# Kernel optimization log

Hardware: AMD Instinct MI355X
Metric: run time of the kernel (lower is better)

The kernel has to match this reference:

```python
import jax, jax.numpy as jnp
import numpy as np

B, S, HID = 2, 2048, 4096
NH, NKV, D = 32, 8, 128  # heads, kv heads, head_dim
GROUPS = NH // NKV
THETA = 10000.0


def _rope_tables():
    inv_freq = 1.0 / (THETA ** (np.arange(0, D, 2, dtype=np.float32) / D))
    pos = np.arange(S, dtype=np.float32)
    freqs = pos[:, None] * inv_freq[None, :]          # [S, D/2]
    emb = np.concatenate([freqs, freqs], axis=-1)      # [S, D]
    cos = np.broadcast_to(np.cos(emb)[None], (B, S, D)).copy()
    sin = np.broadcast_to(np.sin(emb)[None], (B, S, D)).copy()
    return jnp.asarray(cos), jnp.asarray(sin)


def setup_inputs() -> dict:
    key = jax.random.key(0)
    ks = jax.random.split(key, 5)
    hidden_states = jax.random.normal(ks[0], (B, S, HID), dtype=jnp.float32)
    cos, sin = _rope_tables()
    std = 0.02
    Wq = jax.random.normal(ks[1], (NH * D, HID), dtype=jnp.float32) * std
    Wk = jax.random.normal(ks[2], (NKV * D, HID), dtype=jnp.float32) * std
    Wv = jax.random.normal(ks[3], (NKV * D, HID), dtype=jnp.float32) * std
    Wo = jax.random.normal(ks[4], (HID, NH * D), dtype=jnp.float32) * std
    return {"hidden_states": hidden_states, "cos": cos, "sin": sin,
            "Wq": Wq, "Wk": Wk, "Wv": Wv, "Wo": Wo}


def _rotate_half(x):
    x1, x2 = jnp.split(x, 2, axis=-1)
    return jnp.concatenate([-x2, x1], axis=-1)


def reference(hidden_states, cos, sin, Wq, Wk, Wv, Wo):
    b, s, _ = hidden_states.shape
    # QKV projections (no bias; attention_bias=False)
    q = (hidden_states @ Wq.T).reshape(b, s, NH, D).transpose(0, 2, 1, 3)    # [B,NH,S,D]
    k = (hidden_states @ Wk.T).reshape(b, s, NKV, D).transpose(0, 2, 1, 3)   # [B,NKV,S,D]
    v = (hidden_states @ Wv.T).reshape(b, s, NKV, D).transpose(0, 2, 1, 3)
    # RoPE (HF apply_rotary_pos_emb: cos/sin unsqueezed at head dim)
    c = cos[:, None, :, :]
    sn = sin[:, None, :, :]
    q = q * c + _rotate_half(q) * sn
    k = k * c + _rotate_half(k) * sn
    # GQA repeat_kv
    k = jnp.repeat(k, GROUPS, axis=1)                                        # [B,NH,S,D]
    v = jnp.repeat(v, GROUPS, axis=1)
    # dense evalmode: scores + causal mask + fp32 softmax
    scores = jnp.einsum('bhqd,bhkd->bhqk', q, k) / jnp.sqrt(jnp.float32(D))
    causal = jnp.triu(jnp.ones((s, s), dtype=bool), k=1)                     # True above diag
    scores = jnp.where(causal[None, None], jnp.float32(-jnp.inf), scores)
    attn = jax.nn.softmax(scores.astype(jnp.float32), axis=-1).astype(v.dtype)
    out = jnp.einsum('bhqk,bhkd->bhqd', attn, v)                             # [B,NH,S,D]
    out = out.transpose(0, 2, 1, 3).reshape(b, s, NH * D)
    return out @ Wo.T
```

## Files before the change

### kernel.cpp

```cpp
#include <hip/hip_runtime.h>
#include <hip/hip_bf16.h>

#define DEV __device__ __forceinline__

typedef __attribute__((ext_vector_type(8))) short bf16x8;
typedef __attribute__((ext_vector_type(4))) short s16x4;
typedef __attribute__((ext_vector_type(4))) float f32x4;

constexpr int B_ = 2, S_ = 2048, HID_ = 4096, NH_ = 32, NKV_ = 8, D_ = 128;
constexpr int GROUPS_ = NH_ / NKV_;
constexpr float QSCALE_ = 0.08838834764831845f * 1.4426950408889634f;

DEV unsigned short f2bf(float x) {
    union { float f; unsigned int u; } v; v.f = x;
    unsigned int r = v.u + 0x7fffu + ((v.u >> 16) & 1u);
    return (unsigned short)(r >> 16);
}

DEV f32x4 mfma16(bf16x8 a, bf16x8 b, f32x4 c) {
    return __builtin_amdgcn_mfma_f32_16x16x32_bf16(a, b, c, 0, 0, 0);
}

DEV void gll16(const void* g, void* l) {
    __builtin_amdgcn_global_load_lds(
        (const __attribute__((address_space(1))) unsigned int*)g,
        (__attribute__((address_space(3))) unsigned int*)l, 16, 0, 0);
}

__global__ __launch_bounds__(256) void cast_all_k(
    const float* __restrict__ s0, const float* __restrict__ s1,
    const float* __restrict__ s2, const float* __restrict__ s3,
    const float* __restrict__ s4,
    unsigned short* __restrict__ d0, unsigned short* __restrict__ d1,
    unsigned short* __restrict__ d2, unsigned short* __restrict__ d3,
    unsigned short* __restrict__ d4)
{
    int bb = blockIdx.x;
    const float* s; unsigned short* d; int off;
    if      (bb < 8192)  { s = s0; d = d0; off = bb; }
    else if (bb < 16384) { s = s1; d = d1; off = bb - 8192; }
    else if (bb < 18432) { s = s2; d = d2; off = bb - 16384; }
    else if (bb < 20480) { s = s3; d = d3; off = bb - 18432; }
    else                 { s = s4; d = d4; off = bb - 20480; }
    size_t i = ((size_t)off * 256 + threadIdx.x) * 8;
    const f32x4* sp = (const f32x4*)(s + i);
    f32x4 a = sp[0], b = sp[1];
    bf16x8 o;
    o[0] = (short)f2bf(a[0]); o[1] = (short)f2bf(a[1]);
    o[2] = (short)f2bf(a[2]); o[3] = (short)f2bf(a[3]);
    o[4] = (short)f2bf(b[0]); o[5] = (short)f2bf(b[1]);
    o[6] = (short)f2bf(b[2]); o[7] = (short)f2bf(b[3]);
    *(bf16x8*)(d + i) = o;
}

template<int EPI>
__global__ __launch_bounds__(512, 2) void gemm256_k(
    const unsigned short* __restrict__ A, const unsigned short* __restrict__ Bw,
    float* __restrict__ Cf, unsigned short* __restrict__ Qo,
    const float* __restrict__ cosT, const float* __restrict__ sinT,
    int M, int N, int K)
{
    __shared__ __align__(16) unsigned short lds[65536];
    const int tid = threadIdx.x, lane = tid & 63;
    const int w = tid >> 6, wm = w >> 2, wn = w & 3;
    const int la = lane & 15, lb = lane >> 4;

    const int nwg = (int)gridDim.x;
    const int cpx = nwg >> 3;
    const int bid = (int)blockIdx.x;
    const int sw = (bid & 7) * cpx + (bid >> 3);
    const int ntn = N >> 8;
    const int bm = (sw / ntn) << 8, bn = (sw % ntn) << 8;

    const int srow = tid >> 3;
    const int scol8 = (tid & 7) ^ (srow & 7);
    const size_t rK = (size_t)K;
    const unsigned short* gA = A + (size_t)(bm + srow) * rK + scol8 * 8;
    const unsigned short* gB = Bw + (size_t)(bn + srow) * rK + scol8 * 8;

#define STAGE_A_H0(buf, kt) { gll16(gA + (size_t)(kt),            &lds[(buf)*16384 + tid*8]); \
                              gll16(gA + (size_t)(kt) + 128*rK,   &lds[(buf)*16384 + 8192 + tid*8]); }
#define STAGE_A_H1(buf, kt) { gll16(gA + (size_t)(kt) + 64*rK,    &lds[(buf)*16384 + 4096 + tid*8]); \
                              gll16(gA + (size_t)(kt) + 192*rK,   &lds[(buf)*16384 + 12288 + tid*8]); }
#define STAGE_B_H0(buf, kt) { gll16(gB + (size_t)(kt),            &lds[32768 + (buf)*16384 + tid*8]); \
                              gll16(gB + (size_t)(kt) + 64*rK,    &lds[32768 + (buf)*16384 + 4096 + tid*8]); }
#define STAGE_B_H1(buf, kt) { gll16(gB + (size_t)(kt) + 128*rK,   &lds[32768 + (buf)*16384 + 8192 + tid*8]); \
                              gll16(gB + (size_t)(kt) + 192*rK,   &lds[32768 + (buf)*16384 + 12288 + tid*8]); }
#define SB0() __builtin_amdgcn_sched_barrier(0)

    f32x4 acc[8][4];
#pragma unroll
    for (int m = 0; m < 8; ++m)
#pragma unroll
        for (int j = 0; j < 4; ++j) acc[m][j] = f32x4{0.f, 0.f, 0.f, 0.f};

    auto rdA = [&](int buf, int m, int kk) -> bf16x8 {
        int r = wm * 128 + m * 16 + la;
        int slot = (kk * 4 + lb) ^ (la & 7);
        return *(const bf16x8*)&lds[buf * 16384 + r * 64 + slot * 8];
    };
    auto rdB = [&](int buf, int j, int kk) -> bf16x8 {
        int r = (wn + 4 * j) * 16 + la;
        int slot = (kk * 4 + lb) ^ (la & 7);
        return *(const bf16x8*)&lds[32768 + buf * 16384 + r * 64 + slot * 8];
    };

    STAGE_A_H0(0, 0); STAGE_B_H0(0, 0); STAGE_B_H1(0, 0); STAGE_A_H1(0, 0);

    bf16x8 af[4][2], b01[2][2], b23[2][2];
    int cur = 0;
    const int nt = K >> 6;
    for (int t = 0; t < nt; ++t) {
        const bool pre = (t + 1 < nt);
        const int kn = (t + 1) << 6;
        const int nb = cur ^ 1;
        asm volatile("s_waitcnt vmcnt(2)" ::: "memory");
        SB0(); __builtin_amdgcn_s_barrier(); SB0();
#pragma unroll
        for (int m = 0; m < 4; ++m)
#pragma unroll
            for (int kk = 0; kk < 2; ++kk) af[m][kk] = rdA(cur, m, kk);
#pragma unroll
        for (int j = 0; j < 2; ++j)
#pragma unroll
            for (int kk = 0; kk < 2; ++kk) b01[j][kk] = rdB(cur, j, kk);
        if (pre) STAGE_A_H0(nb, kn);
        __builtin_amdgcn_s_setprio(1);
#pragma unroll
        for (int kk = 0; kk < 2; ++kk)
#pragma unroll
            for (int m = 0; m < 4; ++m)
#pragma unroll
                for (int j = 0; j < 2; ++j)
                    acc[m][j] = mfma16(af[m][kk], b01[j][kk], acc[m][j]);
        __builtin_amdgcn_s_setprio(0);
        SB0(); __builtin_amdgcn_s_barrier(); SB0();
#pragma unroll
        for (int j = 0; j < 2; ++j)
#pragma unroll
            for (int kk = 0; kk < 2; ++kk) b23[j][kk] = rdB(cur, j + 2, kk);
        if (pre) STAGE_B_H0(nb, kn);
        __builtin_amdgcn_s_setprio(1);
#pragma unroll
        for (int kk = 0; kk < 2; ++kk)
#pragma unroll
            for (int m = 0; m < 4; ++m)
#pragma unroll
                for (int j = 0; j < 2; ++j)
                    acc[m][j + 2] = mfma16(af[m][kk], b23[j][kk], acc[m][j + 2]);
        __builtin_amdgcn_s_setprio(0);
        if (pre) { asm volatile("s_waitcnt vmcnt(4)" ::: "memory"); }
        else     { asm volatile("s_waitcnt vmcnt(0)" ::: "memory"); }
        SB0(); __builtin_amdgcn_s_barrier(); SB0();
#pragma unroll
        for (int m = 0; m < 4; ++m)
#pragma unroll
            for (int kk = 0; kk < 2; ++kk) af[m][kk] = rdA(cur, m + 4, kk);
        if (pre) STAGE_B_H1(nb, kn);
        __builtin_amdgcn_s_setprio(1);
#pragma unroll
        for (int kk = 0; kk < 2; ++kk)
#pragma unroll
            for (int m = 0; m < 4; ++m)
#pragma unroll
                for (int j = 0; j < 2; ++j)
                    acc[m + 4][j + 2] = mfma16(af[m][kk], b23[j][kk], acc[m + 4][j + 2]);
        __builtin_amdgcn_s_setprio(0);
        SB0(); __builtin_amdgcn_s_barrier(); SB0();
        if (pre) STAGE_A_H1(nb, kn);
        __builtin_amdgcn_s_setprio(1);
#pragma unroll
        for (int kk = 0; kk < 2; ++kk)
#pragma unroll
            for (int m = 0; m < 4; ++m)
#pragma unroll
                for (int j = 0; j < 2; ++j)
                    acc[m + 4][j] = mfma16(af[m][kk], b01[j][kk], acc[m + 4][j]);
        __builtin_amdgcn_s_setprio(0);
        cur ^= 1;
    }
#undef STAGE_A_H0
#undef STAGE_A_H1
#undef STAGE_B_H0
#undef STAGE_B_H1

    const int srow0 = bm + wm * 128;
    if constexpr (EPI == 0) {
#pragma unroll
        for (int m = 0; m < 8; ++m)
#pragma unroll
            for (int j = 0; j < 4; ++j) {
                int col = bn + (wn + 4 * j) * 16 + la;
#pragma unroll
                for (int r = 0; r < 4; ++r)
                    Cf[(size_t)(srow0 + m * 16 + lb * 4 + r) * N + col] = acc[m][j][r];
            }
    } else {
        const int hbase = bn >> 7;
        const int d = wn * 16 + la;
#pragma unroll
        for (int m = 0; m < 8; ++m) {
#pragma unroll
            for (int r = 0; r < 4; ++r) {
                int row = srow0 + m * 16 + lb * 4 + r;
                float cv = cosT[(size_t)row * D_ + d];
                float sv = sinT[(size_t)row * D_ + d];
#pragma unroll
                for (int p = 0; p < 2; ++p) {
                    float x1 = acc[m][p * 2 + 0][r], x2 = acc[m][p * 2 + 1][r];
                    unsigned short* o = Qo + (size_t)row * (NH_ * D_) + (hbase + p) * D_ + d;
                    o[0]  = f2bf((x1 * cv - x2 * sv) * QSCALE_);
                    o[64] = f2bf((x2 * cv + x1 * sv) * QSCALE_);
                }
            }
        }
    }
}

__global__ __launch_bounds__(512, 4) void gemm_kv_k(
    const unsigned short* __restrict__ A, const unsigned short* __restrict__ Bw,
    unsigned short* __restrict__ Ko, unsigned short* __restrict__ Vo,
    const float* __restrict__ cosT, const float* __restrict__ sinT,
    int M, int K)
{
    __shared__ __align__(16) unsigned short lds[32768];
    const int tid = threadIdx.x, lane = tid & 63;
    const int w = tid >> 6, wm = w >> 2, wn = w & 3;
    const int la = lane & 15, lb = lane >> 4;

    const int nwg = (int)gridDim.x;
    const int cpx = nwg >> 3;
    const int bid = (int)blockIdx.x;
    const int sw = (bid & 7) * cpx + (bid >> 3);
    const int ntn = 2048 >> 7;
    const int bm = (sw / ntn) << 7, bn = (sw % ntn) << 7;

    const int srow = tid >> 3;
    const int scol8 = (tid & 7) ^ (srow & 7);
    const size_t rK = (size_t)K;
    const unsigned short* gA = A + (size_t)(bm + srow) * rK + scol8 * 8;
    const unsigned short* gB = Bw + (size_t)(bn + srow) * rK + scol8 * 8;

#define KV_STG_A(buf, kt)  { gll16(gA + (size_t)(kt),          &lds[(buf)*8192 + tid*8]); \
                             gll16(gA + (size_t)(kt) + 64*rK,  &lds[(buf)*8192 + 4096 + tid*8]); }
#define KV_STG_B0(buf, kt)   gll16(gB + (size_t)(kt),          &lds[16384 + (buf)*8192 + tid*8])
#define KV_STG_B1(buf, kt)   gll16(gB + (size_t)(kt) + 64*rK,  &lds[16384 + (buf)*8192 + 4096 + tid*8])
#define SB0() __builtin_amdgcn_sched_barrier(0)

    f32x4 acc[4][2];
#pragma unroll
    for (int m = 0; m < 4; ++m)
#pragma unroll
        for (int j = 0; j < 2; ++j) acc[m][j] = f32x4{0.f, 0.f, 0.f, 0.f};

    auto rdA = [&](int buf, int m, int kk) -> bf16x8 {
        int r = wm * 64 + m * 16 + la;
        int slot = (kk * 4 + lb) ^ (la & 7);
        return *(const bf16x8*)&lds[buf * 8192 + r * 64 + slot * 8];
    };
    auto rdB = [&](int buf, int j, int kk) -> bf16x8 {
        int r = (wn + 4 * j) * 16 + la;
        int slot = (kk * 4 + lb) ^ (la & 7);
        return *(const bf16x8*)&lds[16384 + buf * 8192 + r * 64 + slot * 8];
    };

    KV_STG_A(0, 0); KV_STG_B0(0, 0); KV_STG_B1(0, 0);

    bf16x8 af[4][2], bf0[2], bf1[2];
    int cur = 0;
    const int nt = K >> 6;
    for (int t = 0; t < nt; ++t) {
        const bool pre = (t + 1 < nt);
        const int kn = (t + 1) << 6;
        const int nb = cur ^ 1;
        asm volatile("s_waitcnt vmcnt(1)" ::: "memory");
        SB0(); __builtin_amdgcn_s_barrier(); SB0();
#pragma unroll
        for (int m = 0; m < 4; ++m)
#pragma unroll
            for (int kk = 0; kk < 2; ++kk) af[m][kk] = rdA(cur, m, kk);
#pragma unroll
        for (int kk = 0; kk < 2; ++kk) bf0[kk] = rdB(cur, 0, kk);
        if (pre) { KV_STG_A(nb, kn); KV_STG_B0(nb, kn); }
        __builtin_amdgcn_s_setprio(1);
#pragma unroll
        for (int kk = 0; kk < 2; ++kk)
#pragma unroll
            for (int m = 0; m < 4; ++m)
                acc[m][0] = mfma16(af[m][kk], bf0[kk], acc[m][0]);
        __builtin_amdgcn_s_setprio(0);
        if (pre) { asm volatile("s_waitcnt vmcnt(3)" ::: "memory"); }
        else     { asm volatile("s_waitcnt vmcnt(0)" ::: "memory"); }
        SB0(); __builtin_amdgcn_s_barrier(); SB0();
#pragma unroll
        for (int kk = 0; kk < 2; ++kk) bf1[kk] = rdB(cur, 1, kk);
        if (pre) KV_STG_B1(nb, kn);
        __builtin_amdgcn_s_setprio(1);
#pragma unroll
        for (int kk = 0; kk < 2; ++kk)
#pragma unroll
            for (int m = 0; m < 4; ++m)
                acc[m][1] = mfma16(af[m][kk], bf1[kk], acc[m][1]);
        __builtin_amdgcn_s_setprio(0);
        cur ^= 1;
    }
#undef KV_STG_A
#undef KV_STG_B0
#undef KV_STG_B1
#undef SB0

    const int rbase = bm + wm * 64;
    if (bn < 1024) {
        const int hbase = bn >> 7;
        const int d = wn * 16 + la;
#pragma unroll
        for (int m = 0; m < 4; ++m)
#pragma unroll
            for (int r = 0; r < 4; ++r) {
                int row = rbase + m * 16 + lb * 4 + r;
                float cv = cosT[(size_t)row * D_ + d];
                float sv = sinT[(size_t)row * D_ + d];
                float x1 = acc[m][0][r], x2 = acc[m][1][r];
                unsigned short* o = Ko + (size_t)row * (NKV_ * D_) + hbase * D_ + d;
                o[0]  = f2bf(x1 * cv - x2 * sv);
                o[64] = f2bf(x2 * cv + x1 * sv);
            }
    } else {
        const int kv = (bn - 1024) >> 7;
#pragma unroll
        for (int m = 0; m < 4; ++m) {
            int row = rbase + m * 16 + lb * 4;
            int b = row >> 11, s = row & (S_ - 1);
#pragma unroll
            for (int j = 0; j < 2; ++j) {
                int d = (wn + 4 * j) * 16 + la;
                s16x4 pk;
#pragma unroll
                for (int r = 0; r < 4; ++r) pk[r] = (short)f2bf(acc[m][j][r]);
                *(s16x4*)&Vo[((size_t)(b * NKV_ + kv) * D_ + d) * S_ + s] = pk;
            }
        }
    }
}

template<int EPI, bool ABF16>
__global__ __launch_bounds__(256) void gemm_legacy_k(
    const void* __restrict__ Ap, const float* __restrict__ Bp,
    void* __restrict__ Cp, const float* __restrict__ cosT,
    const float* __restrict__ sinT, int M, int N, int K, float scale)
{
    constexpr int LDT = 40;
    __shared__ __align__(16) unsigned short Asm[128 * LDT];
    __shared__ __align__(16) unsigned short Bsm[128 * LDT];
    const int tid = threadIdx.x;
    const int lane = tid & 63;
    const int w = tid >> 6;
    const int la = lane & 15, lb = lane >> 4;
    const int ntn = N >> 7;
    const int bm = (int)(blockIdx.x / ntn) << 7;
    const int bn = (int)(blockIdx.x % ntn) << 7;

    f32x4 acc[2][8];
#pragma unroll
    for (int i = 0; i < 2; ++i)
#pragma unroll
        for (int j = 0; j < 8; ++j) acc[i][j] = f32x4{0.f, 0.f, 0.f, 0.f};

    for (int kt = 0; kt < K; kt += 32) {
        if constexpr (!ABF16) {
#pragma unroll
            for (int it = 0; it < 4; ++it) {
                int idx = it * 256 + tid;
                int r = idx >> 3, c = (idx & 7) << 2;
                const float* g = (const float*)Ap + (size_t)(bm + r) * K + kt + c;
                f32x4 v = *(const f32x4*)g;
                union { unsigned long long q; unsigned short u[4]; } pk;
                pk.u[0] = f2bf(v[0]); pk.u[1] = f2bf(v[1]);
                pk.u[2] = f2bf(v[2]); pk.u[3] = f2bf(v[3]);
                *(unsigned long long*)&Asm[r * LDT + c] = pk.q;
            }
        } else {
#pragma unroll
            for (int it = 0; it < 2; ++it) {
                int idx = it * 256 + tid;
                int r = idx >> 2, c = (idx & 3) << 3;
                const unsigned short* g =
                    (const unsigned short*)Ap + (size_t)(bm + r) * K + kt + c;
                *(bf16x8*)&Asm[r * LDT + c] = *(const bf16x8*)g;
            }
        }
#pragma unroll
        for (int it = 0; it < 4; ++it) {
            int idx = it * 256 + tid;
            int r = idx >> 3, c = (idx & 7) << 2;
            const float* g = Bp + (size_t)(bn + r) * K + kt + c;
            f32x4 v = *(const f32x4*)g;
            union { unsigned long long q; unsigned short u[4]; } pk;
            pk.u[0] = f2bf(v[0]); pk.u[1] = f2bf(v[1]);
            pk.u[2] = f2bf(v[2]); pk.u[3] = f2bf(v[3]);
            *(unsigned long long*)&Bsm[r * LDT + c] = pk.q;
        }
        __syncthreads();
        bf16x8 af0 = *(bf16x8*)&Asm[(w * 32 + la) * LDT + lb * 8];
        bf16x8 af1 = *(bf16x8*)&Asm[(w * 32 + 16 + la) * LDT + lb * 8];
#pragma unroll
        for (int nb = 0; nb < 8; ++nb) {
            bf16x8 bfr = *(bf16x8*)&Bsm[(nb * 16 + la) * LDT + lb * 8];
            acc[0][nb] = mfma16(af0, bfr, acc[0][nb]);
            acc[1][nb] = mfma16(af1, bfr, acc[1][nb]);
        }
        __syncthreads();
    }

    const int rbase = bm + w * 32;
    if constexpr (EPI == 0) {
        float* C = (float*)Cp;
#pragma unroll
        for (int mf = 0; mf < 2; ++mf)
#pragma unroll
            for (int nb = 0; nb < 8; ++nb)
#pragma unroll
                for (int r = 0; r < 4; ++r)
                    C[(size_t)(rbase + mf * 16 + lb * 4 + r) * N + bn + nb * 16 + la] =
                        acc[mf][nb][r];
    } else if constexpr (EPI == 1) {
        unsigned short* C = (unsigned short*)Cp;
#pragma unroll
        for (int mf = 0; mf < 2; ++mf) {
#pragma unroll
            for (int r = 0; r < 4; ++r) {
                int m = rbase + mf * 16 + lb * 4 + r;
                const float* cb = cosT + (size_t)m * D_;
                const float* sb = sinT + (size_t)m * D_;
#pragma unroll
                for (int nb = 0; nb < 4; ++nb) {
                    int d = nb * 16 + la;
                    float c = cb[d], s = sb[d];
                    float x1 = acc[mf][nb][r], x2 = acc[mf][nb + 4][r];
                    C[(size_t)m * N + bn + d]      = f2bf((x1 * c - x2 * s) * scale);
                    C[(size_t)m * N + bn + d + 64] = f2bf((x2 * c + x1 * s) * scale);
                }
            }
        }
    } else {
        unsigned short* C = (unsigned short*)Cp;
#pragma unroll
        for (int mf = 0; mf < 2; ++mf)
#pragma unroll
            for (int nb = 0; nb < 8; ++nb)
#pragma unroll
                for (int r = 0; r < 4; ++r) {
                    int m = rbase + mf * 16 + lb * 4 + r;
                    int b = m >> 11, s = m & (S_ - 1);
                    int n = bn + nb * 16 + la;
                    int kv = n >> 7, d = n & 127;
                    C[(((size_t)b * NKV_ + kv) * D_ + d) * S_ + s] =
                        f2bf(acc[mf][nb][r]);
                }
    }
}

__global__ __launch_bounds__(256, 2) void attn3_k(
    const unsigned short* __restrict__ Qw,
    const unsigned short* __restrict__ Kw,
    const unsigned short* __restrict__ Vt,
    unsigned short* __restrict__ Ow)
{
    __shared__ __align__(16) unsigned short Ksm[2][64 * 128];
    __shared__ __align__(16) unsigned short Vsm[2][128 * 64];
    const int tid = threadIdx.x, lane = tid & 63, w = tid >> 6;
    const int la = lane & 15, lb = lane >> 4;
    const int blk = blockIdx.x;
    const int qbi = (S_ / 128 - 1) - (blk >> 6);
    const int bh = blk & 63;
    const int b = bh >> 5, h = bh & 31;
    const int kvh = h >> 2;
    const int qb = qbi * 128;
    const int qw0 = qb + w * 32;

    bf16x8 fq[2][4];
    const unsigned short* qp =
        Qw + ((size_t)(b * S_ + qw0 + la) * NH_ + h) * D_ + lb * 8;
#pragma unroll
    for (int mq = 0; mq < 2; ++mq)
#pragma unroll
        for (int kc = 0; kc < 4; ++kc)
            fq[mq][kc] = *(const bf16x8*)(qp + (size_t)mq * 16 * NH_ * D_ + kc * 32);

    float m_[2], l_[2];
    f32x4 oacc[8][2];
    m_[0] = m_[1] = -__builtin_inff();
    l_[0] = l_[1] = 0.f;
#pragma unroll
    for (int db = 0; db < 8; ++db)
#pragma unroll
        for (int mq = 0; mq < 2; ++mq) oacc[db][mq] = f32x4{0.f, 0.f, 0.f, 0.f};

    const int krb = tid >> 4, ksl = tid & 15;
    const int vrb = tid >> 3, vsl = tid & 7;
    const unsigned short* kbase = Kw + ((size_t)b * S_ * NKV_ + kvh) * D_;
    const unsigned short* vbase = Vt + ((size_t)(b * NKV_ + kvh) * D_) * S_;

#define STAGE_KV(buf, kv0) {                                                   \
    _Pragma("unroll")                                                          \
    for (int it = 0; it < 4; ++it) {                                           \
        int row = it * 16 + krb;                                               \
        int cc = ksl ^ (row & 7);                                              \
        gll16(kbase + (size_t)(kv0 + row) * NKV_ * D_ + cc * 8,                \
              &Ksm[buf][(it * 256 + tid) * 8]);                                \
    }                                                                          \
    _Pragma("unroll")                                                          \
    for (int it = 0; it < 4; ++it) {                                           \
        int row = it * 32 + vrb;                                               \
        int cc = vsl ^ (row & 7);                                              \
        gll16(vbase + (size_t)row * S_ + (kv0) + cc * 8,                       \
              &Vsm[buf][(it * 256 + tid) * 8]);                                \
    }                                                                          \
}
#define SB0() __builtin_amdgcn_sched_barrier(0)

    STAGE_KV(0, 0);
    int cur = 0;
    const int ntiles = (qb + 128) >> 6;
    for (int t = 0; t < ntiles; ++t) {
        const int kv0 = t << 6;
        const bool pre = (t + 1 < ntiles);
        if (pre) STAGE_KV(cur ^ 1, kv0 + 64);
        if (pre) { asm volatile("s_waitcnt vmcnt(8)" ::: "memory"); }
        else     { asm volatile("s_waitcnt vmcnt(0)" ::: "memory"); }
        SB0(); __builtin_amdgcn_s_barrier(); SB0();

        if (kv0 < qw0 + 32) {
            f32x4 sacc[4][2];
#pragma unroll
            for (int nk = 0; nk < 4; ++nk)
#pragma unroll
                for (int mq = 0; mq < 2; ++mq) sacc[nk][mq] = f32x4{0.f, 0.f, 0.f, 0.f};
#pragma unroll
            for (int kc = 0; kc < 4; ++kc) {
#pragma unroll
                for (int nk = 0; nk < 4; ++nk) {
                    int row = nk * 16 + la;
                    int slot = (kc * 4 + lb) ^ (la & 7);
                    bf16x8 fk = *(const bf16x8*)&Ksm[cur][row * 128 + slot * 8];
#pragma unroll
                    for (int mq = 0; mq < 2; ++mq)
                        sacc[nk][mq] = mfma16(fk, fq[mq][kc], sacc[nk][mq]);
                }
            }
            const bool diag = (kv0 + 63 > qw0);
            float pv[4][2][4];
            float pm[2];
#pragma unroll
            for (int mq = 0; mq < 2; ++mq) {
                int q = qw0 + mq * 16 + la;
                float mx = -__builtin_inff();
#pragma unroll
                for (int nk = 0; nk < 4; ++nk)
#pragma unroll
                    for (int r = 0; r < 4; ++r) {
                        float s = sacc[nk][mq][r];
                        if (diag) {
                            int k = kv0 + nk * 16 + lb * 4 + r;
                            s = (k <= q) ? s : -__builtin_inff();
                        }
                        pv[nk][mq][r] = s;
                        mx = fmaxf(mx, s);
                    }
                mx = fmaxf(mx, __shfl_xor(mx, 16));
                mx = fmaxf(mx, __shfl_xor(mx, 32));
                pm[mq] = mx;
            }
            const bool upd =
                __any((pm[0] > m_[0] + 8.f) || (pm[1] > m_[1] + 8.f));
            if (upd) {
#pragma unroll
                for (int mq = 0; mq < 2; ++mq) {
                    float mn = fmaxf(m_[mq], pm[mq]);
                    float fac = exp2f(m_[mq] - mn);
                    m_[mq] = mn;
                    l_[mq] *= fac;
#pragma unroll
                    for (int db = 0; db < 8; ++db) oacc[db][mq] *= fac;
                }
            }
            float tsum[2] = {0.f, 0.f};
#pragma unroll
            for (int nk = 0; nk < 4; ++nk)
#pragma unroll
                for (int mq = 0; mq < 2; ++mq)
#pragma unroll
                    for (int r = 0; r < 4; ++r) {
                        float p = exp2f(pv[nk][mq][r] - m_[mq]);
                        pv[nk][mq][r] = p;
                        tsum[mq] += p;
                    }
#pragma unroll
            for (int mq = 0; mq < 2; ++mq) {
                float s = tsum[mq];
                s += __shfl_xor(s, 16);
                s += __shfl_xor(s, 32);
                l_[mq] += s;
            }
            union { bf16x8 v; __hip_bfloat162 h[4]; } fp[2][2];
#pragma unroll
            for (int mq = 0; mq < 2; ++mq)
#pragma unroll
                for (int ks = 0; ks < 2; ++ks) {
                    fp[mq][ks].h[0] = __float22bfloat162_rn(
                        float2{pv[2 * ks][mq][0], pv[2 * ks][mq][1]});
                    fp[mq][ks].h[1] = __float22bfloat162_rn(
                        float2{pv[2 * ks][mq][2], pv[2 * ks][mq][3]});
                    fp[mq][ks].h[2] = __float22bfloat162_rn(
                        float2{pv[2 * ks + 1][mq][0], pv[2 * ks + 1][mq][1]});
                    fp[mq][ks].h[3] = __float22bfloat162_rn(
                        float2{pv[2 * ks + 1][mq][2], pv[2 * ks + 1][mq][3]});
                }
            const int lbh = lb >> 1, lbo = (lb & 1) * 4;
#pragma unroll
            for (int ks = 0; ks < 2; ++ks)
#pragma unroll
                for (int db = 0; db < 8; ++db) {
                    int row = db * 16 + la;
                    int rx = row & 7;
                    const unsigned short* vb = &Vsm[cur][row * 64];
                    s16x4 v0 = *(const s16x4*)&vb[((ks * 4 + lbh) ^ rx) * 8 + lbo];
                    s16x4 v1 = *(const s16x4*)&vb[((ks * 4 + 2 + lbh) ^ rx) * 8 + lbo];
                    bf16x8 fv = __builtin_shufflevector(v0, v1, 0, 1, 2, 3, 4, 5, 6, 7);
#pragma unroll
                    for (int mq = 0; mq < 2; ++mq)
                        oacc[db][mq] = mfma16(fv, fp[mq][ks].v, oacc[db][mq]);
                }
        }
        SB0(); __builtin_amdgcn_s_barrier(); SB0();
        cur ^= 1;
    }
#undef STAGE_KV
#undef SB0

#pragma unroll
    for (int mq = 0; mq < 2; ++mq) {
        float rl = 1.f / l_[mq];
        int q = qw0 + mq * 16 + la;
#pragma unroll
        for (int db = 0; db < 8; ++db) {
            f32x4 o = oacc[db][mq];
            s16x4 pk;
#pragma unroll
            for (int r = 0; r < 4; ++r) pk[r] = (short)f2bf(o[r] * rl);
            int d = db * 16 + lb * 4;
            *(s16x4*)(Ow + (size_t)(b * S_ + q) * (NH_ * D_) + h * D_ + d) = pk;
        }
    }
}

extern "C" void kernel_launch(void* const* d_in, const int* in_sizes, int n_in,
                              void* d_out, int out_size, void* d_ws, size_t ws_size,
                              hipStream_t stream) {
    const float* hs   = (const float*)d_in[0];
    const float* cosT = (const float*)d_in[1];
    const float* sinT = (const float*)d_in[2];
    const float* Wq   = (const float*)d_in[3];
    const float* Wk   = (const float*)d_in[4];
    const float* Wv   = (const float*)d_in[5];
    const float* Wo   = (const float*)d_in[6];

    constexpr size_t Qn  = (size_t)B_ * S_ * NH_ * D_;
    constexpr size_t Kn  = (size_t)B_ * S_ * NKV_ * D_;
    constexpr size_t Hn  = (size_t)B_ * S_ * HID_;
    constexpr size_t Wqn = (size_t)NH_ * D_ * HID_;
    constexpr size_t Wkn = (size_t)NKV_ * D_ * HID_;

    unsigned short* Qws   = (unsigned short*)d_ws;
    unsigned short* Kws   = Qws + Qn;
    unsigned short* Vtws  = Kws + Kn;
    unsigned short* AOws  = Vtws + Kn;
    unsigned short* hsb   = AOws + Qn;
    unsigned short* Wqkvb = hsb + Hn;
    unsigned short* Wob   = Wqkvb + Wqn + 2 * Wkn;
    constexpr size_t need = (Qn + 2 * Kn + Qn + Hn + Wqn + 2 * Wkn + Wqn) * 2;

    const int M = B_ * S_;
    dim3 blk(256);

    if (ws_size >= need) {
        cast_all_k<<<dim3(28672), blk, 0, stream>>>(
            hs, Wq, Wk, Wv, Wo,
            hsb, Wqkvb, Wqkvb + Wqn, Wqkvb + Wqn + Wkn, Wob);

        gemm256_k<1><<<dim3((M / 256) * (HID_ / 256)), dim3(512), 0, stream>>>(
            hsb, Wqkvb, nullptr, Qws, cosT, sinT, M, HID_, HID_);
        gemm_kv_k<<<dim3((M / 128) * (2048 / 128)), dim3(512), 0, stream>>>(
            hsb, Wqkvb + Wqn, Kws, Vtws, cosT, sinT, M, HID_);
        attn3_k<<<dim3(B_ * NH_ * (S_ / 128)), blk, 0, stream>>>(Qws, Kws, Vtws, AOws);
        gemm256_k<0><<<dim3((M / 256) * (HID_ / 256)), dim3(512), 0, stream>>>(
            AOws, Wob, (float*)d_out, nullptr, nullptr, nullptr, M, HID_, NH_ * D_);
    } else {
        unsigned short* Qf = (unsigned short*)d_ws;
        unsigned short* Kf = Qf + Qn;
        unsigned short* Vf = Kf + Kn;
        unsigned short* AOf = Vf + Kn;
        gemm_legacy_k<1, false><<<dim3((M / 128) * (NH_ * D_ / 128)), blk, 0, stream>>>(
            hs, Wq, Qf, cosT, sinT, M, NH_ * D_, HID_, QSCALE_);
        gemm_legacy_k<1, false><<<dim3((M / 128) * (NKV_ * D_ / 128)), blk, 0, stream>>>(
            hs, Wk, Kf, cosT, sinT, M, NKV_ * D_, HID_, 1.0f);
        gemm_legacy_k<3, false><<<dim3((M / 128) * (NKV_ * D_ / 128)), blk, 0, stream>>>(
            hs, Wv, Vf, nullptr, nullptr, M, NKV_ * D_, HID_, 0.f);
        attn3_k<<<dim3(B_ * NH_ * (S_ / 128)), blk, 0, stream>>>(Qf, Kf, Vf, AOf);
        gemm_legacy_k<0, true><<<dim3((M / 128) * (HID_ / 128)), blk, 0, stream>>>(
            AOf, Wo, (float*)d_out, nullptr, nullptr, M, HID_, NH_ * D_, 0.f);
    }
}
```

Before: 474.2 us.

## Enlarge attention blocks to 256 queries with 8 waves and MFMA row sums

```diff
diff --git a/kernel.cpp b/kernel.cpp
--- a/kernel.cpp
+++ b/kernel.cpp
@@ -25,6 +25,10 @@
     __builtin_amdgcn_global_load_lds(
         (const __attribute__((address_space(1))) unsigned int*)g,
         (__attribute__((address_space(3))) unsigned int*)l, 16, 0, 0);
+}
+
+DEV int vperm(int s) {
+    return (s & ~31) | (((s >> 2) & 3) << 3) | (((s >> 4) & 1) << 2) | (s & 3);
 }
 
 __global__ __launch_bounds__(256) void cast_all_k(
@@ -331,13 +335,14 @@
         for (int m = 0; m < 4; ++m) {
             int row = rbase + m * 16 + lb * 4;
             int b = row >> 11, s = row & (S_ - 1);
+            int sp = vperm(s);
 #pragma unroll
             for (int j = 0; j < 2; ++j) {
                 int d = (wn + 4 * j) * 16 + la;
                 s16x4 pk;
 #pragma unroll
                 for (int r = 0; r < 4; ++r) pk[r] = (short)f2bf(acc[m][j][r]);
-                *(s16x4*)&Vo[((size_t)(b * NKV_ + kv) * D_ + d) * S_ + s] = pk;
+                *(s16x4*)&Vo[((size_t)(b * NKV_ + kv) * D_ + d) * S_ + sp] = pk;
             }
         }
     }
@@ -454,13 +459,13 @@
                     int b = m >> 11, s = m & (S_ - 1);
                     int n = bn + nb * 16 + la;
                     int kv = n >> 7, d = n & 127;
-                    C[(((size_t)b * NKV_ + kv) * D_ + d) * S_ + s] =
+                    C[(((size_t)b * NKV_ + kv) * D_ + d) * S_ + vperm(s)] =
                         f2bf(acc[mf][nb][r]);
                 }
     }
 }
 
-__global__ __launch_bounds__(256, 2) void attn3_k(
+__global__ __launch_bounds__(512, 4) void attn4_k(
     const unsigned short* __restrict__ Qw,
     const unsigned short* __restrict__ Kw,
     const unsigned short* __restrict__ Vt,
@@ -471,11 +476,12 @@
     const int tid = threadIdx.x, lane = tid & 63, w = tid >> 6;
     const int la = lane & 15, lb = lane >> 4;
     const int blk = blockIdx.x;
-    const int qbi = (S_ / 128 - 1) - (blk >> 6);
+    const int g = blk >> 6;
+    const int qbi = (g < 4) ? (7 - g) : (g - 4);
     const int bh = blk & 63;
     const int b = bh >> 5, h = bh & 31;
     const int kvh = h >> 2;
-    const int qb = qbi * 128;
+    const int qb = qbi * 256;
     const int qw0 = qb + w * 32;
 
     bf16x8 fq[2][4];
@@ -487,10 +493,14 @@
         for (int kc = 0; kc < 4; ++kc)
             fq[mq][kc] = *(const bf16x8*)(qp + (size_t)mq * 16 * NH_ * D_ + kc * 32);
 
-    float m_[2], l_[2];
-    f32x4 oacc[8][2];
+    bf16x8 ones;
+#pragma unroll
+    for (int i = 0; i < 8; ++i) ones[i] = (short)0x3F80;
+
+    float m_[2];
+    f32x4 oacc[8][2], lacc[2];
     m_[0] = m_[1] = -__builtin_inff();
-    l_[0] = l_[1] = 0.f;
+    lacc[0] = lacc[1] = f32x4{0.f, 0.f, 0.f, 0.f};
 #pragma unroll
     for (int db = 0; db < 8; ++db)
 #pragma unroll
@@ -503,30 +513,30 @@
 
 #define STAGE_KV(buf, kv0) {                                                   \
     _Pragma("unroll")                                                          \
-    for (int it = 0; it < 4; ++it) {                                           \
-        int row = it * 16 + krb;                                               \
+    for (int it = 0; it < 2; ++it) {                                           \
+        int row = it * 32 + krb;                                               \
         int cc = ksl ^ (row & 7);                                              \
         gll16(kbase + (size_t)(kv0 + row) * NKV_ * D_ + cc * 8,                \
-              &Ksm[buf][(it * 256 + tid) * 8]);                                \
+              &Ksm[buf][(it * 512 + tid) * 8]);                                \
     }                                                                          \
     _Pragma("unroll")                                                          \
-    for (int it = 0; it < 4; ++it) {                                           \
-        int row = it * 32 + vrb;                                               \
+    for (int it = 0; it < 2; ++it) {                                           \
+        int row = it * 64 + vrb;                                               \
         int cc = vsl ^ (row & 7);                                              \
         gll16(vbase + (size_t)row * S_ + (kv0) + cc * 8,                       \
-              &Vsm[buf][(it * 256 + tid) * 8]);                                \
+              &Vsm[buf][(it * 512 + tid) * 8]);                                \
     }                                                                          \
 }
 #define SB0() __builtin_amdgcn_sched_barrier(0)
 
     STAGE_KV(0, 0);
     int cur = 0;
-    const int ntiles = (qb + 128) >> 6;
+    const int ntiles = (qb + 256) >> 6;
     for (int t = 0; t < ntiles; ++t) {
         const int kv0 = t << 6;
         const bool pre = (t + 1 < ntiles);
         if (pre) STAGE_KV(cur ^ 1, kv0 + 64);
-        if (pre) { asm volatile("s_waitcnt vmcnt(8)" ::: "memory"); }
+        if (pre) { asm volatile("s_waitcnt vmcnt(4)" ::: "memory"); }
         else     { asm volatile("s_waitcnt vmcnt(0)" ::: "memory"); }
         SB0(); __builtin_amdgcn_s_barrier(); SB0();
 
@@ -579,29 +589,18 @@
                     float mn = fmaxf(m_[mq], pm[mq]);
                     float fac = exp2f(m_[mq] - mn);
                     m_[mq] = mn;
-                    l_[mq] *= fac;
+                    lacc[mq] *= fac;
 #pragma unroll
                     for (int db = 0; db < 8; ++db) oacc[db][mq] *= fac;
                 }
             }
-            float tsum[2] = {0.f, 0.f};
 #pragma unroll
             for (int nk = 0; nk < 4; ++nk)
 #pragma unroll
                 for (int mq = 0; mq < 2; ++mq)
 #pragma unroll
-                    for (int r = 0; r < 4; ++r) {
-                        float p = exp2f(pv[nk][mq][r] - m_[mq]);
-                        pv[nk][mq][r] = p;
-                        tsum[mq] += p;
-                    }
-#pragma unroll
-            for (int mq = 0; mq < 2; ++mq) {
-                float s = tsum[mq];
-                s += __shfl_xor(s, 16);
-                s += __shfl_xor(s, 32);
-                l_[mq] += s;
-            }
+                    for (int r = 0; r < 4; ++r)
+                        pv[nk][mq][r] = exp2f(pv[nk][mq][r] - m_[mq]);
             union { bf16x8 v; __hip_bfloat162 h[4]; } fp[2][2];
 #pragma unroll
             for (int mq = 0; mq < 2; ++mq)
@@ -616,21 +615,21 @@
                     fp[mq][ks].h[3] = __float22bfloat162_rn(
                         float2{pv[2 * ks + 1][mq][2], pv[2 * ks + 1][mq][3]});
                 }
-            const int lbh = lb >> 1, lbo = (lb & 1) * 4;
-#pragma unroll
-            for (int ks = 0; ks < 2; ++ks)
+#pragma unroll
+            for (int ks = 0; ks < 2; ++ks) {
 #pragma unroll
                 for (int db = 0; db < 8; ++db) {
                     int row = db * 16 + la;
-                    int rx = row & 7;
-                    const unsigned short* vb = &Vsm[cur][row * 64];
-                    s16x4 v0 = *(const s16x4*)&vb[((ks * 4 + lbh) ^ rx) * 8 + lbo];
-                    s16x4 v1 = *(const s16x4*)&vb[((ks * 4 + 2 + lbh) ^ rx) * 8 + lbo];
-                    bf16x8 fv = __builtin_shufflevector(v0, v1, 0, 1, 2, 3, 4, 5, 6, 7);
+                    int slot = (ks * 4 + lb) ^ (row & 7);
+                    bf16x8 fv = *(const bf16x8*)&Vsm[cur][row * 64 + slot * 8];
 #pragma unroll
                     for (int mq = 0; mq < 2; ++mq)
                         oacc[db][mq] = mfma16(fv, fp[mq][ks].v, oacc[db][mq]);
                 }
+#pragma unroll
+                for (int mq = 0; mq < 2; ++mq)
+                    lacc[mq] = mfma16(ones, fp[mq][ks].v, lacc[mq]);
+            }
         }
         SB0(); __builtin_amdgcn_s_barrier(); SB0();
         cur ^= 1;
@@ -640,7 +639,7 @@
 
 #pragma unroll
     for (int mq = 0; mq < 2; ++mq) {
-        float rl = 1.f / l_[mq];
+        float rl = 1.f / lacc[mq][0];
         int q = qw0 + mq * 16 + la;
 #pragma unroll
         for (int db = 0; db < 8; ++db) {
@@ -692,7 +691,8 @@
             hsb, Wqkvb, nullptr, Qws, cosT, sinT, M, HID_, HID_);
         gemm_kv_k<<<dim3((M / 128) * (2048 / 128)), dim3(512), 0, stream>>>(
             hsb, Wqkvb + Wqn, Kws, Vtws, cosT, sinT, M, HID_);
-        attn3_k<<<dim3(B_ * NH_ * (S_ / 128)), blk, 0, stream>>>(Qws, Kws, Vtws, AOws);
+        attn4_k<<<dim3(B_ * NH_ * (S_ / 256)), dim3(512), 0, stream>>>(
+            Qws, Kws, Vtws, AOws);
         gemm256_k<0><<<dim3((M / 256) * (HID_ / 256)), dim3(512), 0, stream>>>(
             AOws, Wob, (float*)d_out, nullptr, nullptr, nullptr, M, HID_, NH_ * D_);
     } else {
@@ -706,7 +706,8 @@
             hs, Wk, Kf, cosT, sinT, M, NKV_ * D_, HID_, 1.0f);
         gemm_legacy_k<3, false><<<dim3((M / 128) * (NKV_ * D_ / 128)), blk, 0, stream>>>(
             hs, Wv, Vf, nullptr, nullptr, M, NKV_ * D_, HID_, 0.f);
-        attn3_k<<<dim3(B_ * NH_ * (S_ / 128)), blk, 0, stream>>>(Qf, Kf, Vf, AOf);
+        attn4_k<<<dim3(B_ * NH_ * (S_ / 256)), dim3(512), 0, stream>>>(
+            Qf, Kf, Vf, AOf);
         gemm_legacy_k<0, true><<<dim3((M / 128) * (HID_ / 128)), blk, 0, stream>>>(
             AOf, Wo, (float*)d_out, nullptr, nullptr, M, HID_, NH_ * D_, 0.f);
     }
```

Result: slower. 714.3 us (+50.6%).
